# Optimization experiments

Hardware: AMD Instinct MI355X
Metric: run time of the kernel (lower is better)

The kernel has to match this reference:

```python
import jax, jax.numpy as jnp
import numpy as np

B, L, D, H = 4, 1024, 768, 12
HD = D // H  # head_dim = 64
SCALING = HD ** -0.5


def setup_inputs() -> dict:
    key = jax.random.key(0)
    ks = jax.random.split(key, 6)
    x = jax.random.normal(ks[0], (B, L, D), dtype=jnp.float32)
    attn_bias = jax.random.normal(ks[1], (B, H, L, L), dtype=jnp.float32)
    s_in = 1.0 / np.sqrt(D)
    w_in = jax.random.uniform(ks[2], (3 * D, D), dtype=jnp.float32, minval=-s_in, maxval=s_in)
    b_in = jax.random.uniform(ks[3], (3 * D,), dtype=jnp.float32, minval=-s_in, maxval=s_in)
    w_out = jax.random.uniform(ks[4], (D, D), dtype=jnp.float32, minval=-s_in, maxval=s_in)
    b_out = jax.random.uniform(ks[5], (D,), dtype=jnp.float32, minval=-s_in, maxval=s_in)
    return {"x": x, "attn_bias": attn_bias, "w_in": w_in, "b_in": b_in,
            "w_out": w_out, "b_out": b_out}


def reference(x, attn_bias, w_in, b_in, w_out, b_out):
    # fused QKV projection: [B, L, 3D]
    qkv = jnp.einsum('bld,ed->ble', x, w_in) + b_in
    q, k, v = jnp.split(qkv, 3, axis=-1)
    # [B, H, L, HD]
    q = q.reshape(B, L, H, HD).transpose(0, 2, 1, 3) * SCALING
    k = k.reshape(B, L, H, HD).transpose(0, 2, 1, 3)
    v = v.reshape(B, L, H, HD).transpose(0, 2, 1, 3)
    # bias-augmented attention scores: [B, H, L, L]
    scores = jnp.einsum('bhqd,bhkd->bhqk', q, k) + attn_bias
    probs = jax.nn.softmax(scores, axis=-1)
    # attend: [B, H, L, HD] -> [B, L, D]
    o = jnp.einsum('bhqk,bhkd->bhqd', probs, v)
    o = o.transpose(0, 2, 1, 3).reshape(B, L, D)
    return jnp.einsum('bld,ed->ble', o, w_out) + b_out
```

## Files before the change

kernel.cpp:

```cpp
#include <hip/hip_runtime.h>
#include <hip/hip_bf16.h>
#include <stdint.h>

#define B_ 4
#define L_ 1024
#define D_ 768
#define H_ 12
#define HD_ 64
#define M_ 4096
#define N3_ 2304

typedef float f32x4 __attribute__((ext_vector_type(4)));
typedef float f32x4v __attribute__((ext_vector_type(4)));
typedef short bf16x8 __attribute__((ext_vector_type(8)));
typedef unsigned short u16;
typedef u16 u16x8 __attribute__((ext_vector_type(8)));
typedef u16 u16x4 __attribute__((ext_vector_type(4)));
typedef uint32_t u32x2 __attribute__((ext_vector_type(2)));

#define AS3 __attribute__((address_space(3)))
#define AS1 __attribute__((address_space(1)))

__device__ __forceinline__ void gll16(const void* g, void* l) {
  __builtin_amdgcn_global_load_lds((const AS1 void*)g, (AS3 void*)l, 16, 0, 0);
}

__device__ __forceinline__ u16 f2bf(float f) {
  uint32_t u = __builtin_bit_cast(uint32_t, f);
  u += 0x7fffu + ((u >> 16) & 1u);
  return (u16)(u >> 16);
}

__global__ void k_cvt3(const float* __restrict__ a, u16* __restrict__ ao, int na4,
                       const float* __restrict__ b, u16* __restrict__ bo, int nb4,
                       const float* __restrict__ c, u16* __restrict__ co, int nc4) {
  int i = blockIdx.x * 256 + threadIdx.x;
  const float* src;
  u16* dst;
  if (i < na4) {
    src = a; dst = ao;
  } else if (i < na4 + nb4) {
    src = b; dst = bo; i -= na4;
  } else if (i < na4 + nb4 + nc4) {
    src = c; dst = co; i -= na4 + nb4;
  } else {
    return;
  }
  f32x4v v = ((const f32x4v*)src)[i];
  u16x4 o;
  o.x = f2bf(v.x); o.y = f2bf(v.y); o.z = f2bf(v.z); o.w = f2bf(v.w);
  ((u16x4*)dst)[i] = o;
}

__global__ __launch_bounds__(256) void k_gemm_qkv(
    const u16* __restrict__ Xb, const u16* __restrict__ Wb,
    const float* __restrict__ b_in,
    u16* __restrict__ gQ, u16* __restrict__ gK, u16* __restrict__ gV) {
  __shared__ u16 As[128 * 64];
  __shared__ u16 Bs[128 * 64];
  const int tid = threadIdx.x;
  const int lane = tid & 63;
  const int w = tid >> 6;
  const int wm = (w >> 1) * 64;
  const int wn = (w & 1) * 64;
  const int lr = lane & 15;
  const int lg = lane >> 4;
  const int m0 = blockIdx.x * 128;
  const int n0 = blockIdx.y * 128;

  f32x4 acc[4][4];
#pragma unroll
  for (int i = 0; i < 4; ++i)
#pragma unroll
    for (int j = 0; j < 4; ++j) acc[i][j] = (f32x4){0.f, 0.f, 0.f, 0.f};

  for (int kt = 0; kt < 12; ++kt) {
    __syncthreads();
#pragma unroll
    for (int i = 0; i < 4; ++i) {
      int seg = i * 256 + tid;
      int row = seg >> 3;
      int sl = (seg & 7) ^ (row & 7);
      gll16(Xb + (size_t)(m0 + row) * 768 + kt * 64 + sl * 8, (char*)As + seg * 16);
      gll16(Wb + (size_t)(n0 + row) * 768 + kt * 64 + sl * 8, (char*)Bs + seg * 16);
    }
    __syncthreads();
#pragma unroll
    for (int kh = 0; kh < 2; ++kh) {
      bf16x8 af[4], bfr[4];
#pragma unroll
      for (int t = 0; t < 4; ++t) {
        int ra = wm + t * 16 + lr;
        af[t] = *(const bf16x8*)((const char*)As + ra * 128 +
                                 ((kh * 64 + lg * 16) ^ ((ra & 7) << 4)));
        int rb = wn + t * 16 + lr;
        bfr[t] = *(const bf16x8*)((const char*)Bs + rb * 128 +
                                  ((kh * 64 + lg * 16) ^ ((rb & 7) << 4)));
      }
#pragma unroll
      for (int mi = 0; mi < 4; ++mi)
#pragma unroll
        for (int ni = 0; ni < 4; ++ni)
          acc[mi][ni] = __builtin_amdgcn_mfma_f32_16x16x32_bf16(
              af[mi], bfr[ni], acc[mi][ni], 0, 0, 0);
    }
  }
  const int sec = blockIdx.y / 6;
  u16* dst = sec == 0 ? gQ : (sec == 1 ? gK : gV);
  const float scale = sec == 0 ? 0.125f : 1.0f;
#pragma unroll
  for (int ni = 0; ni < 4; ++ni) {
    int e = n0 + wn + ni * 16 + lr;
    float bias = b_in[e];
    int es = e - sec * 768;
    int h = es >> 6, d = es & 63;
#pragma unroll
    for (int mi = 0; mi < 4; ++mi) {
#pragma unroll
      for (int j = 0; j < 4; ++j) {
        int m = m0 + wm + mi * 16 + lg * 4 + j;
        int bb = m >> 10, lq = m & 1023;
        float vv = (acc[mi][ni][j] + bias) * scale;
        dst[(size_t)((bb * 12 + h) * 1024 + lq) * 64 + d] = f2bf(vv);
      }
    }
  }
}

__global__ __launch_bounds__(256) void k_transpose(const u16* __restrict__ V,
                                                   u16* __restrict__ Vt) {
  __shared__ u16 t[64][66];
  const int tid = threadIdx.x;
  const int bh = blockIdx.x >> 4;
  const int kv0 = (blockIdx.x & 15) * 64;
  {
    int r = tid >> 2, c0 = (tid & 3) * 16;
    const u16* src = V + (size_t)(bh * 1024 + kv0 + r) * 64 + c0;
#pragma unroll
    for (int p = 0; p < 2; ++p) {
      u16x8 x = *(const u16x8*)(src + p * 8);
#pragma unroll
      for (int e = 0; e < 8; ++e) t[r][c0 + p * 8 + e] = x[e];
    }
  }
  __syncthreads();
  {
    int d = tid >> 2, k0 = (tid & 3) * 16;
    u16* dst = Vt + (size_t)(bh * 64 + d) * 1024 + kv0 + k0;
#pragma unroll
    for (int p = 0; p < 2; ++p) {
      u16x8 o;
#pragma unroll
      for (int e = 0; e < 8; ++e) o[e] = t[k0 + p * 8 + e][d];
      *(u16x8*)(dst + p * 8) = o;
    }
  }
}

__global__ __launch_bounds__(256) void k_attn(
    const u16* __restrict__ gQ, const u16* __restrict__ gK,
    const u16* __restrict__ gVt, const float* __restrict__ gBias,
    u16* __restrict__ gO) {
  __shared__ u16 Ks[2][64 * 64];
  __shared__ u16 Vs[2][64 * 64];
  __shared__ f32x4 PlV[4][128];
  const int tid = threadIdx.x;
  const int lane = tid & 63;
  const int w = tid >> 6;
  const int lr = lane & 15;
  const int lg = lane >> 4;
  const int lb = (blockIdx.x & 7) * 96 + (blockIdx.x >> 3);
  const int bh = lb >> 4;
  const int q0 = (lb & 15) * 64;
  const int qr = q0 + w * 16;

#define STAGE_KV(buf, kv0)                                                     \
  do {                                                                         \
    _Pragma("unroll") for (int i_ = 0; i_ < 2; ++i_) {                         \
      int seg_ = i_ * 256 + tid;                                               \
      int row_ = seg_ >> 3;                                                    \
      int sl_ = (seg_ & 7) ^ (row_ & 7);                                       \
      gll16(gK + (size_t)(bh * 1024 + (kv0) + row_) * 64 + sl_ * 8,            \
            (char*)Ks[buf] + seg_ * 16);                                       \
      gll16(gVt + (size_t)(bh * 64 + row_) * 1024 + (kv0) + sl_ * 8,           \
            (char*)Vs[buf] + seg_ * 16);                                       \
    }                                                                          \
  } while (0)

#define BIAS_LOAD(dst, kv0)                                                    \
  do {                                                                         \
    _Pragma("unroll") for (int ni_ = 0; ni_ < 4; ++ni_) {                      \
      dst[ni_] = __builtin_nontemporal_load(                                   \
          (const f32x4*)(bline + (kv0) + ni_ * 16 + lg * 4));                  \
    }                                                                          \
  } while (0)

  const float* bline = gBias + (size_t)(bh * 1024 + qr + lr) * 1024;

  bf16x8 qa[2];
#pragma unroll
  for (int kh = 0; kh < 2; ++kh)
    qa[kh] = *(const bf16x8*)(gQ + (size_t)(bh * 1024 + qr + lr) * 64 + kh * 32 + lg * 8);

  f32x4 oacc[4];
#pragma unroll
  for (int dt = 0; dt < 4; ++dt) oacc[dt] = (f32x4){0.f, 0.f, 0.f, 0.f};
  float mrow = -1e30f, lrow = 0.f;

  char* plw = (char*)PlV[w];
  const int swz = (lr & 7) << 4;

  STAGE_KV(0, 0);
  f32x4 bcur[4], bnext[4];
  BIAS_LOAD(bcur, 0);
  BIAS_LOAD(bnext, 64);
  asm volatile("s_waitcnt vmcnt(8)" ::: "memory");
  __builtin_amdgcn_s_barrier();

#pragma unroll 2
  for (int t = 0; t < 16; ++t) {
    const int cur = t & 1;

    if (t < 15) STAGE_KV(cur ^ 1, (t + 1) * 64);
    f32x4 bn[4];
    if (t < 14) BIAS_LOAD(bn, (t + 2) * 64);

    f32x4 s[4];
#pragma unroll
    for (int ni = 0; ni < 4; ++ni) s[ni] = (f32x4){0.f, 0.f, 0.f, 0.f};
    __builtin_amdgcn_s_setprio(1);
#pragma unroll
    for (int kh = 0; kh < 2; ++kh)
#pragma unroll
      for (int ni = 0; ni < 4; ++ni) {
        int rk = ni * 16 + lr;
        bf16x8 kb = *(const bf16x8*)((const char*)Ks[cur] + rk * 128 +
                                     ((kh * 64 + lg * 16) ^ ((rk & 7) << 4)));
        s[ni] = __builtin_amdgcn_mfma_f32_16x16x32_bf16(kb, qa[kh], s[ni], 0, 0, 0);
      }
    __builtin_amdgcn_s_setprio(0);

#pragma unroll
    for (int ni = 0; ni < 4; ++ni) s[ni] += bcur[ni];

    float mx0 = fmaxf(fmaxf(s[0][0], s[0][1]), fmaxf(s[0][2], s[0][3]));
    float mx1 = fmaxf(fmaxf(s[1][0], s[1][1]), fmaxf(s[1][2], s[1][3]));
    float mx2 = fmaxf(fmaxf(s[2][0], s[2][1]), fmaxf(s[2][2], s[2][3]));
    float mx3 = fmaxf(fmaxf(s[3][0], s[3][1]), fmaxf(s[3][2], s[3][3]));
    float vmax = fmaxf(fmaxf(mx0, mx1), fmaxf(mx2, mx3));
    vmax = fmaxf(vmax, __shfl_xor(vmax, 16));
    vmax = fmaxf(vmax, __shfl_xor(vmax, 32));
    float mnew = fmaxf(mrow, vmax);
    float al = __expf(mrow - mnew);
    mrow = mnew;
#pragma unroll
    for (int ni = 0; ni < 4; ++ni)
#pragma unroll
      for (int j = 0; j < 4; ++j) s[ni][j] = __expf(s[ni][j] - mnew);
    float r0 = (s[0][0] + s[0][1]) + (s[0][2] + s[0][3]);
    float r1 = (s[1][0] + s[1][1]) + (s[1][2] + s[1][3]);
    float r2 = (s[2][0] + s[2][1]) + (s[2][2] + s[2][3]);
    float r3 = (s[3][0] + s[3][1]) + (s[3][2] + s[3][3]);
    float rs = (r0 + r1) + (r2 + r3);
    rs += __shfl_xor(rs, 16);
    rs += __shfl_xor(rs, 32);
    lrow = lrow * al + rs;

    f32x4 av;
#pragma unroll
    for (int j = 0; j < 4; ++j) av[j] = __shfl(al, (lane & 48) | (lg * 4 + j));
#pragma unroll
    for (int dt = 0; dt < 4; ++dt) oacc[dt] *= av;

#pragma unroll
    for (int ni = 0; ni < 4; ++ni) {
      uint32_t w0 = (uint32_t)f2bf(s[ni][0]) | ((uint32_t)f2bf(s[ni][1]) << 16);
      uint32_t w1 = (uint32_t)f2bf(s[ni][2]) | ((uint32_t)f2bf(s[ni][3]) << 16);
      u32x2 pv = {w0, w1};
      *(u32x2*)(plw + lr * 128 + ((ni * 32 + lg * 8) ^ swz)) = pv;
    }
    __builtin_amdgcn_s_setprio(1);
#pragma unroll
    for (int kh = 0; kh < 2; ++kh) {
      bf16x8 pa = *(const bf16x8*)(plw + lr * 128 + ((kh * 64 + lg * 16) ^ swz));
#pragma unroll
      for (int dt = 0; dt < 4; ++dt) {
        int rv = dt * 16 + lr;
        bf16x8 vb = *(const bf16x8*)((const char*)Vs[cur] + rv * 128 +
                                     ((kh * 64 + lg * 16) ^ ((rv & 7) << 4)));
        oacc[dt] = __builtin_amdgcn_mfma_f32_16x16x32_bf16(pa, vb, oacc[dt], 0, 0, 0);
      }
    }
    __builtin_amdgcn_s_setprio(0);

    if (t < 14) {
#pragma unroll
      for (int z = 0; z < 4; ++z) { bcur[z] = bnext[z]; bnext[z] = bn[z]; }
    } else {
#pragma unroll
      for (int z = 0; z < 4; ++z) bcur[z] = bnext[z];
    }

    if (t < 14) {
      asm volatile("s_waitcnt vmcnt(4) lgkmcnt(0)" ::: "memory");
      __builtin_amdgcn_s_barrier();
    } else if (t < 15) {
      asm volatile("s_waitcnt vmcnt(0) lgkmcnt(0)" ::: "memory");
      __builtin_amdgcn_s_barrier();
    }
  }

  float inv = 1.0f / lrow;
  f32x4 iv;
#pragma unroll
  for (int j = 0; j < 4; ++j) iv[j] = __shfl(inv, (lane & 48) | (lg * 4 + j));
  const int bg = bh / 12, h = bh % 12;
#pragma unroll
  for (int j = 0; j < 4; ++j) {
    int row = qr + lg * 4 + j;
#pragma unroll
    for (int dt = 0; dt < 4; ++dt) {
      gO[(size_t)(bg * 1024 + row) * 768 + h * 64 + dt * 16 + lr] =
          f2bf(oacc[dt][j] * iv[j]);
    }
  }
#undef STAGE_KV
#undef BIAS_LOAD
}

__global__ __launch_bounds__(256) void k_gemm_out(
    const u16* __restrict__ Ob, const u16* __restrict__ Wb,
    const float* __restrict__ b_out, float* __restrict__ out) {
  __shared__ u16 As[64 * 64];
  __shared__ u16 Bs[64 * 64];
  const int tid = threadIdx.x;
  const int lane = tid & 63;
  const int w = tid >> 6;
  const int wm = (w >> 1) * 32;
  const int wn = (w & 1) * 32;
  const int lr = lane & 15;
  const int lg = lane >> 4;
  const int m0 = blockIdx.x * 64;
  const int n0 = blockIdx.y * 64;

  f32x4 acc[2][2];
#pragma unroll
  for (int i = 0; i < 2; ++i)
#pragma unroll
    for (int j = 0; j < 2; ++j) acc[i][j] = (f32x4){0.f, 0.f, 0.f, 0.f};

  for (int kt = 0; kt < 12; ++kt) {
    __syncthreads();
#pragma unroll
    for (int i = 0; i < 2; ++i) {
      int seg = i * 256 + tid;
      int row = seg >> 3;
      int sl = (seg & 7) ^ (row & 7);
      gll16(Ob + (size_t)(m0 + row) * 768 + kt * 64 + sl * 8, (char*)As + seg * 16);
      gll16(Wb + (size_t)(n0 + row) * 768 + kt * 64 + sl * 8, (char*)Bs + seg * 16);
    }
    __syncthreads();
#pragma unroll
    for (int kh = 0; kh < 2; ++kh) {
      bf16x8 af[2], bfr[2];
#pragma unroll
      for (int t = 0; t < 2; ++t) {
        int ra = wm + t * 16 + lr;
        af[t] = *(const bf16x8*)((const char*)As + ra * 128 +
                                 ((kh * 64 + lg * 16) ^ ((ra & 7) << 4)));
        int rb = wn + t * 16 + lr;
        bfr[t] = *(const bf16x8*)((const char*)Bs + rb * 128 +
                                  ((kh * 64 + lg * 16) ^ ((rb & 7) << 4)));
      }
#pragma unroll
      for (int mi = 0; mi < 2; ++mi)
#pragma unroll
        for (int ni = 0; ni < 2; ++ni)
          acc[mi][ni] = __builtin_amdgcn_mfma_f32_16x16x32_bf16(
              af[mi], bfr[ni], acc[mi][ni], 0, 0, 0);
    }
  }
#pragma unroll
  for (int ni = 0; ni < 2; ++ni) {
    int n = n0 + wn + ni * 16 + lr;
    float bias = b_out[n];
#pragma unroll
    for (int mi = 0; mi < 2; ++mi) {
#pragma unroll
      for (int j = 0; j < 4; ++j) {
        int m = m0 + wm + mi * 16 + lg * 4 + j;
        out[(size_t)m * 768 + n] = acc[mi][ni][j] + bias;
      }
    }
  }
}

extern "C" void kernel_launch(void* const* d_in, const int* in_sizes, int n_in,
                              void* d_out, int out_size, void* d_ws, size_t ws_size,
                              hipStream_t stream) {
  const float* x = (const float*)d_in[0];
  const float* attn_bias = (const float*)d_in[1];
  const float* w_in = (const float*)d_in[2];
  const float* b_in = (const float*)d_in[3];
  const float* w_out = (const float*)d_in[4];
  const float* b_out = (const float*)d_in[5];
  float* out = (float*)d_out;

  char* ws = (char*)d_ws;
  size_t off = 0;
  u16* xb = (u16*)(ws + off);  off += (size_t)M_ * D_ * 2;
  u16* wib = (u16*)(ws + off); off += (size_t)N3_ * D_ * 2;
  u16* wob = (u16*)(ws + off); off += (size_t)D_ * D_ * 2;
  u16* q = (u16*)(ws + off);   off += (size_t)48 * 1024 * 64 * 2;
  u16* k = (u16*)(ws + off);   off += (size_t)48 * 1024 * 64 * 2;
  u16* v = (u16*)(ws + off);   off += (size_t)48 * 1024 * 64 * 2;
  u16* vt = (u16*)(ws + off);  off += (size_t)48 * 1024 * 64 * 2;
  u16* ob = (u16*)(ws + off);  off += (size_t)M_ * D_ * 2;

  const int na4 = (M_ * D_) / 4;
  const int nb4 = (N3_ * D_) / 4;
  const int nc4 = (D_ * D_) / 4;
  k_cvt3<<<(na4 + nb4 + nc4 + 255) / 256, 256, 0, stream>>>(
      x, xb, na4, w_in, wib, nb4, w_out, wob, nc4);
  k_gemm_qkv<<<dim3(32, 18), 256, 0, stream>>>(xb, wib, b_in, q, k, v);
  k_transpose<<<768, 256, 0, stream>>>(v, vt);
  k_attn<<<768, 256, 0, stream>>>(q, k, vt, attn_bias, ob);
  k_gemm_out<<<dim3(64, 12), 256, 0, stream>>>(ob, wob, b_out, out);
}
```

Measured before the change: 125.3 us.

## Stage attention bias tiles through LDS via async global_load_lds

```diff
diff --git a/kernel.cpp b/kernel.cpp
--- a/kernel.cpp
+++ b/kernel.cpp
@@ -163,6 +163,7 @@
     u16* __restrict__ gO) {
   __shared__ u16 Ks[2][64 * 64];
   __shared__ u16 Vs[2][64 * 64];
+  __shared__ float Bi[2][64 * 64];
   __shared__ f32x4 PlV[4][128];
   const int tid = threadIdx.x;
   const int lane = tid & 63;
@@ -174,7 +175,7 @@
   const int q0 = (lb & 15) * 64;
   const int qr = q0 + w * 16;
 
-#define STAGE_KV(buf, kv0)                                                     \
+#define STAGE(buf, kv0)                                                        \
   do {                                                                         \
     _Pragma("unroll") for (int i_ = 0; i_ < 2; ++i_) {                         \
       int seg_ = i_ * 256 + tid;                                               \
@@ -185,18 +186,15 @@
       gll16(gVt + (size_t)(bh * 64 + row_) * 1024 + (kv0) + sl_ * 8,           \
             (char*)Vs[buf] + seg_ * 16);                                       \
     }                                                                          \
-  } while (0)
-
-#define BIAS_LOAD(dst, kv0)                                                    \
-  do {                                                                         \
-    _Pragma("unroll") for (int ni_ = 0; ni_ < 4; ++ni_) {                      \
-      dst[ni_] = __builtin_nontemporal_load(                                   \
-          (const f32x4*)(bline + (kv0) + ni_ * 16 + lg * 4));                  \
+    _Pragma("unroll") for (int i_ = 0; i_ < 4; ++i_) {                         \
+      int seg_ = i_ * 256 + tid;                                               \
+      int qrow_ = seg_ >> 4;                                                   \
+      int c_ = (seg_ & 15) ^ (qrow_ & 7);                                      \
+      gll16(gBias + (size_t)(bh * 1024 + q0 + qrow_) * 1024 + (kv0) + c_ * 4,  \
+            (char*)Bi[buf] + seg_ * 16);                                       \
     }                                                                          \
   } while (0)
 
-  const float* bline = gBias + (size_t)(bh * 1024 + qr + lr) * 1024;
-
   bf16x8 qa[2];
 #pragma unroll
   for (int kh = 0; kh < 2; ++kh)
@@ -210,20 +208,12 @@
   char* plw = (char*)PlV[w];
   const int swz = (lr & 7) << 4;
 
-  STAGE_KV(0, 0);
-  f32x4 bcur[4], bnext[4];
-  BIAS_LOAD(bcur, 0);
-  BIAS_LOAD(bnext, 64);
-  asm volatile("s_waitcnt vmcnt(8)" ::: "memory");
-  __builtin_amdgcn_s_barrier();
-
-#pragma unroll 2
+  STAGE(0, 0);
+  __syncthreads();
+
   for (int t = 0; t < 16; ++t) {
     const int cur = t & 1;
-
-    if (t < 15) STAGE_KV(cur ^ 1, (t + 1) * 64);
-    f32x4 bn[4];
-    if (t < 14) BIAS_LOAD(bn, (t + 2) * 64);
+    if (t < 15) STAGE(cur ^ 1, (t + 1) * 64);
 
     f32x4 s[4];
 #pragma unroll
@@ -241,7 +231,11 @@
     __builtin_amdgcn_s_setprio(0);
 
 #pragma unroll
-    for (int ni = 0; ni < 4; ++ni) s[ni] += bcur[ni];
+    for (int ni = 0; ni < 4; ++ni) {
+      f32x4 bv = *(const f32x4*)((const char*)Bi[cur] + (w * 16 + lr) * 256 +
+                                 (((ni * 4 + lg) ^ (lr & 7)) << 4));
+      s[ni] += bv;
+    }
 
     float mx0 = fmaxf(fmaxf(s[0][0], s[0][1]), fmaxf(s[0][2], s[0][3]));
     float mx1 = fmaxf(fmaxf(s[1][0], s[1][1]), fmaxf(s[1][2], s[1][3]));
@@ -293,21 +287,7 @@
     }
     __builtin_amdgcn_s_setprio(0);
 
-    if (t < 14) {
-#pragma unroll
-      for (int z = 0; z < 4; ++z) { bcur[z] = bnext[z]; bnext[z] = bn[z]; }
-    } else {
-#pragma unroll
-      for (int z = 0; z < 4; ++z) bcur[z] = bnext[z];
-    }
-
-    if (t < 14) {
-      asm volatile("s_waitcnt vmcnt(4) lgkmcnt(0)" ::: "memory");
-      __builtin_amdgcn_s_barrier();
-    } else if (t < 15) {
-      asm volatile("s_waitcnt vmcnt(0) lgkmcnt(0)" ::: "memory");
-      __builtin_amdgcn_s_barrier();
-    }
+    __syncthreads();
   }
 
   float inv = 1.0f / lrow;
@@ -324,8 +304,7 @@
           f2bf(oacc[dt][j] * iv[j]);
     }
   }
-#undef STAGE_KV
-#undef BIAS_LOAD
+#undef STAGE
 }
 
 __global__ __launch_bounds__(256) void k_gemm_out(
```

Result: faster. 121.8 us (-2.8%).
